# Performance work log

Measured on AMD Instinct MI355X. Metric: run time of the kernel, lower is better.

The kernel has to match this reference:

```python
import jax, jax.numpy as jnp
import numpy as np

B, D, OUT, K = 2048, 256, 256, 16


def setup_inputs() -> dict:
    key = jax.random.key(0)
    k1, k2, k3, k4 = jax.random.split(key, 4)
    x = jax.random.normal(k1, (B, D), dtype=jnp.float32)
    values = jax.random.uniform(k2, (OUT, D, K), dtype=jnp.float32, minval=-0.05, maxval=0.05)
    skip_w = jax.random.normal(k3, (OUT, D), dtype=jnp.float32) * (1.0 / np.sqrt(D).astype(np.float32))
    skip_b = jax.random.normal(k4, (OUT,), dtype=jnp.float32) * 0.01
    return {"x": x, "values": values, "skip_w": skip_w, "skip_b": skip_b}


def reference(x, values, skip_w, skip_b):
    # x: (B, D); values: (OUT, D, K); skip_w: (OUT, D); skip_b: (OUT,)
    num_knots = values.shape[-1]
    grid = jnp.linspace(-1.0, 1.0, num_knots)  # (K,)
    xc = jnp.clip(x, -1.0, 1.0)
    # torch.bucketize(x, grid) with right=False == searchsorted side='left'
    right = jnp.searchsorted(grid, xc, side='left')
    left = jnp.clip(right - 1, 0, num_knots - 2)  # (B, D)
    right = left + 1
    g0 = grid[left]
    g1 = grid[right]
    w = (xc - g0) / (g1 - g0 + 1e-12)  # (B, D)
    # Gather spline values per (sample, input-dim) knot bucket.
    vt = jnp.transpose(values, (1, 2, 0))  # (D, K, OUT)
    dim_idx = jnp.arange(xc.shape[1])[None, :]  # (1, D)
    v_left = vt[dim_idx, left]    # (B, D, OUT)
    v_right = vt[dim_idx, right]  # (B, D, OUT)
    # Linear interpolation + sum over input dims.
    y = jnp.sum((1.0 - w)[..., None] * v_left + w[..., None] * v_right, axis=1)  # (B, OUT)
    # Skip connection on the clamped input (torch reassigns x = clamp(x) first).
    return y + xc @ skip_w.T + skip_b
```

## Files before the change

### kernel.cpp

```cpp
#include <hip/hip_runtime.h>
#include <hip/hip_bf16.h>


namespace {
constexpr int Bsz  = 2048;
constexpr int Din  = 256;
constexpr int Dout = 256;
constexpr int Kn   = 16;
constexpr int KKNOT = Din * Kn;
constexpr int Ksp   = KKNOT + Din;
constexpr int KB    = Ksp / 32;
constexpr int KBK   = KKNOT / 32;
constexpr float INV_H = 7.5f;
constexpr float Hgrid = 2.0f / 15.0f;

constexpr int NSPLIT = 9;
constexpr int SPSK   = 16;
constexpr int SPSS   = 8;
constexpr int PELEM  = Bsz * Dout;
constexpr int SXS    = 36;
}

typedef __attribute__((ext_vector_type(8))) short shortx8;
typedef __attribute__((ext_vector_type(4))) float floatx4;

__device__ __forceinline__ unsigned int f2bf(float f) {
  __hip_bfloat16 h = __float2bfloat16(f);
  return (unsigned int)*reinterpret_cast<unsigned short*>(&h);
}
__device__ __forceinline__ float clamp1(float v) {
  return fminf(1.f, fmaxf(-1.f, v));
}
__device__ __forceinline__ unsigned int packbf(unsigned int e0, unsigned int e1) {
  return (e1 & 0xffff0000u) | (e0 >> 16);
}
__device__ __forceinline__ unsigned int rnd(float f) {
  return __float_as_uint(f) + 0x8000u;
}

__global__ __launch_bounds__(256) void kan_prep(
    const float* __restrict__ values, const float* __restrict__ skip_w,
    unsigned short* __restrict__ Wf) {
  const int tid = blockIdx.x * 256 + threadIdx.x;
  const int q  = tid & 3;
  const int n  = (tid >> 2) & 15;
  const int og = (tid >> 6) & 15;
  const int kb = tid >> 10;
  const int o  = og * 16 + n;
  const int k0 = kb * 32 + q * 8;
  const float* src = (kb < KBK)
      ? values + (size_t)o * KKNOT + k0
      : skip_w + (size_t)o * Din + (k0 - KKNOT);
  const float4 v0 = *(const float4*)src;
  const float4 v1 = *(const float4*)(src + 4);
  const size_t chunk = (size_t)kb * 1024 + og * 64 + q * 16 + n;
  *(uint4*)(Wf + chunk * 8) = make_uint4(
      f2bf(v0.x) | (f2bf(v0.y) << 16), f2bf(v0.z) | (f2bf(v0.w) << 16),
      f2bf(v1.x) | (f2bf(v1.y) << 16), f2bf(v1.z) | (f2bf(v1.w) << 16));
}

__global__ __launch_bounds__(256) void kan_gemm(
    const float* __restrict__ x, const unsigned short* __restrict__ Wf,
    float* __restrict__ part) {
  __shared__ float sx[32 * SXS];
  __shared__ __align__(16) unsigned short aLds[2][32 * 32];

  const int tid  = threadIdx.x;
  const int wave = tid >> 6, lane = tid & 63;
  const int ks   = blockIdx.x % NSPLIT;
  const int mi   = blockIdx.x / NSPLIT;
  const int m0   = mi * 32;
  const int og0  = wave * 4;
  const int lrow = lane & 15, lq = lane >> 4;

  const int brow = tid >> 3;
  const int bseg = tid & 7;
  const float h0 = (float)((bseg & 3) * 4);
  const int   bds = bseg >> 2;

  const uint4* B = (const uint4*)Wf;

  floatx4 acc[2][4] = {};
  uint4 bb[2][4];

  if (ks < 8) {
    const int kb0 = ks * SPSK;
    const int d0  = ks * 32;
    {
      const float4 v = *(const float4*)(x + (size_t)(m0 + brow) * Din + d0 + bseg * 4);
      *(float4*)&sx[brow * SXS + bseg * 4] = v;
    }
    __syncthreads();

    #pragma unroll
    for (int j = 0; j < 4; ++j)
      bb[0][j] = B[(size_t)kb0 * 1024 + (og0 + j) * 64 + lane];
    {
      const float xv = sx[brow * SXS + 0 + bds];
      const float t  = (clamp1(xv) + 1.f) * INV_H;
      unsigned int e0 = rnd(fmaxf(0.f, 1.f - fabsf(t - h0)));
      unsigned int e1 = rnd(fmaxf(0.f, 1.f - fabsf(t - (h0 + 1.f))));
      unsigned int e2 = rnd(fmaxf(0.f, 1.f - fabsf(t - (h0 + 2.f))));
      unsigned int e3 = rnd(fmaxf(0.f, 1.f - fabsf(t - (h0 + 3.f))));
      *(uint2*)&aLds[0][brow * 32 + bseg * 4] =
          make_uint2(packbf(e0, e1), packbf(e2, e3));
    }

    for (int s = 0; s < SPSK; ++s) {
      const int cur = s & 1, nxt = cur ^ 1;
      if (s + 1 < SPSK) {
        #pragma unroll
        for (int j = 0; j < 4; ++j)
          bb[nxt][j] = B[(size_t)(kb0 + s + 1) * 1024 + (og0 + j) * 64 + lane];
      }
      __syncthreads();

      if (s + 1 < SPSK) {
        const float xv = sx[brow * SXS + 2 * (s + 1) + bds];
        const float t  = (clamp1(xv) + 1.f) * INV_H;
        unsigned int e0 = rnd(fmaxf(0.f, 1.f - fabsf(t - h0)));
        unsigned int e1 = rnd(fmaxf(0.f, 1.f - fabsf(t - (h0 + 1.f))));
        unsigned int e2 = rnd(fmaxf(0.f, 1.f - fabsf(t - (h0 + 2.f))));
        unsigned int e3 = rnd(fmaxf(0.f, 1.f - fabsf(t - (h0 + 3.f))));
        *(uint2*)&aLds[nxt][brow * 32 + bseg * 4] =
            make_uint2(packbf(e0, e1), packbf(e2, e3));
      }

      shortx8 af[2];
      #pragma unroll
      for (int i = 0; i < 2; ++i)
        af[i] = *(const shortx8*)&aLds[cur][(16 * i + lrow) * 32 + lq * 8];
      #pragma unroll
      for (int j = 0; j < 4; ++j) {
        union { uint4 u; shortx8 s; } bc;
        bc.u = bb[cur][j];
        #pragma unroll
        for (int i = 0; i < 2; ++i)
          acc[i][j] = __builtin_amdgcn_mfma_f32_16x16x32_bf16(af[i], bc.s, acc[i][j], 0, 0, 0);
      }
    }
  } else {
    const int kb0 = KBK;
    float4 px[2];
    #pragma unroll
    for (int j = 0; j < 4; ++j)
      bb[0][j] = B[(size_t)kb0 * 1024 + (og0 + j) * 64 + lane];
    px[0] = *(const float4*)(x + (size_t)(m0 + brow) * Din + bseg * 4);
    {
      *(uint2*)&aLds[0][brow * 32 + bseg * 4] = make_uint2(
          packbf(rnd(clamp1(px[0].x)), rnd(clamp1(px[0].y))),
          packbf(rnd(clamp1(px[0].z)), rnd(clamp1(px[0].w))));
    }

    for (int s = 0; s < SPSS; ++s) {
      const int cur = s & 1, nxt = cur ^ 1;
      if (s + 1 < SPSS) {
        #pragma unroll
        for (int j = 0; j < 4; ++j)
          bb[nxt][j] = B[(size_t)(kb0 + s + 1) * 1024 + (og0 + j) * 64 + lane];
        px[nxt] = *(const float4*)(x + (size_t)(m0 + brow) * Din + (s + 1) * 32 + bseg * 4);
      }
      __syncthreads();

      if (s + 1 < SPSS) {
        *(uint2*)&aLds[nxt][brow * 32 + bseg * 4] = make_uint2(
            packbf(rnd(clamp1(px[nxt].x)), rnd(clamp1(px[nxt].y))),
            packbf(rnd(clamp1(px[nxt].z)), rnd(clamp1(px[nxt].w))));
      }

      shortx8 af[2];
      #pragma unroll
      for (int i = 0; i < 2; ++i)
        af[i] = *(const shortx8*)&aLds[cur][(16 * i + lrow) * 32 + lq * 8];
      #pragma unroll
      for (int j = 0; j < 4; ++j) {
        union { uint4 u; shortx8 s; } bc;
        bc.u = bb[cur][j];
        #pragma unroll
        for (int i = 0; i < 2; ++i)
          acc[i][j] = __builtin_amdgcn_mfma_f32_16x16x32_bf16(af[i], bc.s, acc[i][j], 0, 0, 0);
      }
    }
  }

  const int wtile = mi * 4 + wave;
  float* P = part + (size_t)ks * PELEM + (size_t)wtile * 2048;
  #pragma unroll
  for (int i = 0; i < 2; ++i)
    #pragma unroll
    for (int j = 0; j < 4; ++j)
      *(floatx4*)&P[((i * 4 + j) * 64 + lane) * 4] = acc[i][j];
}

__global__ __launch_bounds__(256) void kan_reduce(
    const float* __restrict__ part, const float* __restrict__ skip_b,
    float* __restrict__ out) {
  const int tid = blockIdx.x * 256 + threadIdx.x;
  float4 a = make_float4(0.f, 0.f, 0.f, 0.f);
  #pragma unroll
  for (int s = 0; s < NSPLIT; ++s) {
    const float4 p = *(const float4*)(part + (size_t)s * PELEM + (size_t)tid * 4);
    a.x += p.x; a.y += p.y; a.z += p.z; a.w += p.w;
  }
  const int f4    = tid & 511, wtile = tid >> 9;
  const int ij    = f4 >> 6,  lane  = f4 & 63;
  const int i     = ij >> 2,  j     = ij & 3;
  const int mi    = wtile >> 2;
  const int wave  = wtile & 3;
  const int b0    = mi * 32 + 16 * i + (lane >> 4) * 4;
  const int o     = wave * 64 + 16 * j + (lane & 15);
  const float sb  = skip_b[o];
  out[(size_t)(b0 + 0) * Dout + o] = a.x + sb;
  out[(size_t)(b0 + 1) * Dout + o] = a.y + sb;
  out[(size_t)(b0 + 2) * Dout + o] = a.z + sb;
  out[(size_t)(b0 + 3) * Dout + o] = a.w + sb;
}

__device__ __forceinline__ void knot_interp(float xraw, float& xv, float& w, int& l) {
  xv = fminf(1.0f, fmaxf(-1.0f, xraw));
  float t = (xv + 1.0f) * INV_H;
  l = (int)ceilf(t) - 1;
  l = l < 0 ? 0 : (l > Kn - 2 ? Kn - 2 : l);
  float g0 = -1.0f + Hgrid * (float)l;
  w = (xv - g0) * INV_H;
}

__global__ __launch_bounds__(256) void prep_transpose(
    const float* __restrict__ values, const float* __restrict__ skip_w,
    float* __restrict__ vt, float* __restrict__ swt) {
  int idx = blockIdx.x * blockDim.x + threadIdx.x;
  if (idx < Din * Kn * Dout) {
    int k = idx & (Kn - 1);
    int d = (idx >> 4) & (Din - 1);
    int o = idx >> 12;
    vt[(d * Kn + k) * Dout + o] = values[idx];
  }
  if (idx < Dout * Din) {
    int d = idx & (Din - 1);
    int o = idx >> 8;
    swt[d * Dout + o] = skip_w[idx];
  }
}

__global__ __launch_bounds__(256) void kan_main(
    const float* __restrict__ x, const float* __restrict__ vt,
    const float* __restrict__ swt, const float* __restrict__ skip_b,
    float* __restrict__ out) {
  __shared__ float s_w[4][Din];
  __shared__ float s_x[4][Din];
  __shared__ int   s_l[4][Din];
  const int tid = threadIdx.x;
  const int b0  = blockIdx.x * 4;
  for (int i = tid; i < 4 * Din; i += 256) {
    int bb = i >> 8;
    int d  = i & (Din - 1);
    float xv, w; int l;
    knot_interp(x[(b0 + bb) * Din + d], xv, w, l);
    s_w[bb][d] = w; s_x[bb][d] = xv; s_l[bb][d] = l;
  }
  __syncthreads();
  const int g = tid >> 6, lane = tid & 63;
  const int o = lane << 2, b = b0 + g;
  float4 acc = make_float4(0.f, 0.f, 0.f, 0.f);
  for (int d = 0; d < Din; ++d) {
    const float w = s_w[g][d], xv = s_x[g][d];
    const int l = s_l[g][d];
    const float* base = vt + (d * Kn + l) * Dout + o;
    const float4 vl = *(const float4*)(base);
    const float4 vr = *(const float4*)(base + Dout);
    const float4 sw = *(const float4*)(swt + d * Dout + o);
    acc.x = fmaf(xv, sw.x, fmaf(w, vr.x - vl.x, acc.x + vl.x));
    acc.y = fmaf(xv, sw.y, fmaf(w, vr.y - vl.y, acc.y + vl.y));
    acc.z = fmaf(xv, sw.z, fmaf(w, vr.z - vl.z, acc.z + vl.z));
    acc.w = fmaf(xv, sw.w, fmaf(w, vr.w - vl.w, acc.w + vl.w));
  }
  const float4 bias = *(const float4*)(skip_b + o);
  acc.x += bias.x; acc.y += bias.y; acc.z += bias.z; acc.w += bias.w;
  *(float4*)(out + (size_t)b * Dout + o) = acc;
}

extern "C" void kernel_launch(void* const* d_in, const int* in_sizes, int n_in,
                              void* d_out, int out_size, void* d_ws, size_t ws_size,
                              hipStream_t stream) {
  (void)in_sizes; (void)n_in; (void)out_size;
  const float* x      = (const float*)d_in[0];
  const float* values = (const float*)d_in[1];
  const float* skip_w = (const float*)d_in[2];
  const float* skip_b = (const float*)d_in[3];
  float* out = (float*)d_out;

  const size_t wf_bytes   = (size_t)Dout * Ksp * sizeof(unsigned short);
  const size_t part_bytes = (size_t)NSPLIT * PELEM * sizeof(float);
  const size_t need_gemm  = wf_bytes + part_bytes;
  const size_t need_fb    = (size_t)(Din * Kn * Dout + Din * Dout) * sizeof(float);

  if (ws_size >= need_gemm) {
    unsigned short* Wf = (unsigned short*)d_ws;
    float* part = (float*)((char*)d_ws + wf_bytes);
    kan_prep<<<(KB * 1024) / 256, 256, 0, stream>>>(values, skip_w, Wf);
    kan_gemm<<<(Bsz / 32) * NSPLIT, 256, 0, stream>>>(x, Wf, part);
    kan_reduce<<<PELEM / 4 / 256, 256, 0, stream>>>(part, skip_b, out);
  } else if (ws_size >= need_fb) {
    float* vt  = (float*)d_ws;
    float* swt = vt + Din * Kn * Dout;
    prep_transpose<<<(Din * Kn * Dout + 255) / 256, 256, 0, stream>>>(values, skip_w, vt, swt);
    kan_main<<<Bsz / 4, 256, 0, stream>>>(x, vt, swt, skip_b, out);
  }
}
```

Before: 78.24 us.

## Halve GEMM row tile and cut split-K count to reduce partial traffic

The row tile per block shrinks from 32 to 16 and the K split drops from 9 to 5, so each spline slice now covers 64 input dims. Each thread builds two hat-basis entries instead of four, and each wave issues one MFMA row tile instead of two. The aim is to shrink the partial-sum buffer written and reduced (fewer splits) while keeping the block count similar. The cost is that each weight tile loaded is reused across half as many rows, which raises weight bandwidth per output, and each K loop is longer.

```diff
diff --git a/kernel.cpp b/kernel.cpp
--- a/kernel.cpp
+++ b/kernel.cpp
@@ -14,11 +14,11 @@
 constexpr float INV_H = 7.5f;
 constexpr float Hgrid = 2.0f / 15.0f;
 
-constexpr int NSPLIT = 9;
-constexpr int SPSK   = 16;
+constexpr int NSPLIT = 5;
+constexpr int SPSK   = 32;
 constexpr int SPSS   = 8;
 constexpr int PELEM  = Bsz * Dout;
-constexpr int SXS    = 36;
+constexpr int SXS    = 68;
 }
 
 typedef __attribute__((ext_vector_type(8))) short shortx8;
@@ -62,33 +62,33 @@
 __global__ __launch_bounds__(256) void kan_gemm(
     const float* __restrict__ x, const unsigned short* __restrict__ Wf,
     float* __restrict__ part) {
-  __shared__ float sx[32 * SXS];
-  __shared__ __align__(16) unsigned short aLds[2][32 * 32];
+  __shared__ float sx[16 * SXS];
+  __shared__ __align__(16) unsigned short aLds[2][16 * 32];
 
   const int tid  = threadIdx.x;
   const int wave = tid >> 6, lane = tid & 63;
   const int ks   = blockIdx.x % NSPLIT;
   const int mi   = blockIdx.x / NSPLIT;
-  const int m0   = mi * 32;
+  const int m0   = mi * 16;
   const int og0  = wave * 4;
   const int lrow = lane & 15, lq = lane >> 4;
 
-  const int brow = tid >> 3;
-  const int bseg = tid & 7;
-  const float h0 = (float)((bseg & 3) * 4);
-  const int   bds = bseg >> 2;
+  const int brow  = tid >> 4;
+  const int bcol2 = tid & 15;
+  const int dsel  = bcol2 >> 3;
+  const float h0  = (float)(2 * (bcol2 & 7));
 
   const uint4* B = (const uint4*)Wf;
 
-  floatx4 acc[2][4] = {};
+  floatx4 acc[4] = {};
   uint4 bb[2][4];
 
-  if (ks < 8) {
+  if (ks < 4) {
     const int kb0 = ks * SPSK;
-    const int d0  = ks * 32;
+    const int d0  = ks * 64;
     {
-      const float4 v = *(const float4*)(x + (size_t)(m0 + brow) * Din + d0 + bseg * 4);
-      *(float4*)&sx[brow * SXS + bseg * 4] = v;
+      const float4 v = *(const float4*)(x + (size_t)(m0 + brow) * Din + d0 + bcol2 * 4);
+      *(float4*)&sx[brow * SXS + bcol2 * 4] = v;
     }
     __syncthreads();
 
@@ -96,14 +96,11 @@
     for (int j = 0; j < 4; ++j)
       bb[0][j] = B[(size_t)kb0 * 1024 + (og0 + j) * 64 + lane];
     {
-      const float xv = sx[brow * SXS + 0 + bds];
+      const float xv = sx[brow * SXS + dsel];
       const float t  = (clamp1(xv) + 1.f) * INV_H;
-      unsigned int e0 = rnd(fmaxf(0.f, 1.f - fabsf(t - h0)));
-      unsigned int e1 = rnd(fmaxf(0.f, 1.f - fabsf(t - (h0 + 1.f))));
-      unsigned int e2 = rnd(fmaxf(0.f, 1.f - fabsf(t - (h0 + 2.f))));
-      unsigned int e3 = rnd(fmaxf(0.f, 1.f - fabsf(t - (h0 + 3.f))));
-      *(uint2*)&aLds[0][brow * 32 + bseg * 4] =
-          make_uint2(packbf(e0, e1), packbf(e2, e3));
+      const unsigned int e0 = rnd(fmaxf(0.f, 1.f - fabsf(t - h0)));
+      const unsigned int e1 = rnd(fmaxf(0.f, 1.f - fabsf(t - (h0 + 1.f))));
+      *(unsigned int*)&aLds[0][brow * 32 + 2 * bcol2] = packbf(e0, e1);
     }
 
     for (int s = 0; s < SPSK; ++s) {
@@ -116,41 +113,30 @@
       __syncthreads();
 
       if (s + 1 < SPSK) {
-        const float xv = sx[brow * SXS + 2 * (s + 1) + bds];
+        const float xv = sx[brow * SXS + 2 * (s + 1) + dsel];
         const float t  = (clamp1(xv) + 1.f) * INV_H;
-        unsigned int e0 = rnd(fmaxf(0.f, 1.f - fabsf(t - h0)));
-        unsigned int e1 = rnd(fmaxf(0.f, 1.f - fabsf(t - (h0 + 1.f))));
-        unsigned int e2 = rnd(fmaxf(0.f, 1.f - fabsf(t - (h0 + 2.f))));
-        unsigned int e3 = rnd(fmaxf(0.f, 1.f - fabsf(t - (h0 + 3.f))));
-        *(uint2*)&aLds[nxt][brow * 32 + bseg * 4] =
-            make_uint2(packbf(e0, e1), packbf(e2, e3));
-      }
-
-      shortx8 af[2];
-      #pragma unroll
-      for (int i = 0; i < 2; ++i)
-        af[i] = *(const shortx8*)&aLds[cur][(16 * i + lrow) * 32 + lq * 8];
+        const unsigned int e0 = rnd(fmaxf(0.f, 1.f - fabsf(t - h0)));
+        const unsigned int e1 = rnd(fmaxf(0.f, 1.f - fabsf(t - (h0 + 1.f))));
+        *(unsigned int*)&aLds[nxt][brow * 32 + 2 * bcol2] = packbf(e0, e1);
+      }
+
+      const shortx8 af = *(const shortx8*)&aLds[cur][lrow * 32 + lq * 8];
       #pragma unroll
       for (int j = 0; j < 4; ++j) {
         union { uint4 u; shortx8 s; } bc;
         bc.u = bb[cur][j];
-        #pragma unroll
-        for (int i = 0; i < 2; ++i)
-          acc[i][j] = __builtin_amdgcn_mfma_f32_16x16x32_bf16(af[i], bc.s, acc[i][j], 0, 0, 0);
+        acc[j] = __builtin_amdgcn_mfma_f32_16x16x32_bf16(af, bc.s, acc[j], 0, 0, 0);
       }
     }
   } else {
     const int kb0 = KBK;
-    float4 px[2];
+    float2 px[2];
     #pragma unroll
     for (int j = 0; j < 4; ++j)
       bb[0][j] = B[(size_t)kb0 * 1024 + (og0 + j) * 64 + lane];
-    px[0] = *(const float4*)(x + (size_t)(m0 + brow) * Din + bseg * 4);
-    {
-      *(uint2*)&aLds[0][brow * 32 + bseg * 4] = make_uint2(
-          packbf(rnd(clamp1(px[0].x)), rnd(clamp1(px[0].y))),
-          packbf(rnd(clamp1(px[0].z)), rnd(clamp1(px[0].w))));
-    }
+    px[0] = *(const float2*)(x + (size_t)(m0 + brow) * Din + 2 * bcol2);
+    *(unsigned int*)&aLds[0][brow * 32 + 2 * bcol2] =
+        packbf(rnd(clamp1(px[0].x)), rnd(clamp1(px[0].y)));
 
     for (int s = 0; s < SPSS; ++s) {
       const int cur = s & 1, nxt = cur ^ 1;
@@ -158,38 +144,30 @@
         #pragma unroll
         for (int j = 0; j < 4; ++j)
           bb[nxt][j] = B[(size_t)(kb0 + s + 1) * 1024 + (og0 + j) * 64 + lane];
-        px[nxt] = *(const float4*)(x + (size_t)(m0 + brow) * Din + (s + 1) * 32 + bseg * 4);
+        px[nxt] = *(const float2*)(x + (size_t)(m0 + brow) * Din + (s + 1) * 32 + 2 * bcol2);
       }
       __syncthreads();
 
       if (s + 1 < SPSS) {
-        *(uint2*)&aLds[nxt][brow * 32 + bseg * 4] = make_uint2(
-            packbf(rnd(clamp1(px[nxt].x)), rnd(clamp1(px[nxt].y))),
-            packbf(rnd(clamp1(px[nxt].z)), rnd(clamp1(px[nxt].w))));
-      }
-
-      shortx8 af[2];
-      #pragma unroll
-      for (int i = 0; i < 2; ++i)
-        af[i] = *(const shortx8*)&aLds[cur][(16 * i + lrow) * 32 + lq * 8];
+        *(unsigned int*)&aLds[nxt][brow * 32 + 2 * bcol2] =
+            packbf(rnd(clamp1(px[nxt].x)), rnd(clamp1(px[nxt].y)));
+      }
+
+      const shortx8 af = *(const shortx8*)&aLds[cur][lrow * 32 + lq * 8];
       #pragma unroll
       for (int j = 0; j < 4; ++j) {
         union { uint4 u; shortx8 s; } bc;
         bc.u = bb[cur][j];
-        #pragma unroll
-        for (int i = 0; i < 2; ++i)
-          acc[i][j] = __builtin_amdgcn_mfma_f32_16x16x32_bf16(af[i], bc.s, acc[i][j], 0, 0, 0);
+        acc[j] = __builtin_amdgcn_mfma_f32_16x16x32_bf16(af, bc.s, acc[j], 0, 0, 0);
       }
     }
   }
 
   const int wtile = mi * 4 + wave;
-  float* P = part + (size_t)ks * PELEM + (size_t)wtile * 2048;
+  float* P = part + (size_t)ks * PELEM + (size_t)wtile * 1024;
   #pragma unroll
-  for (int i = 0; i < 2; ++i)
-    #pragma unroll
-    for (int j = 0; j < 4; ++j)
-      *(floatx4*)&P[((i * 4 + j) * 64 + lane) * 4] = acc[i][j];
+  for (int j = 0; j < 4; ++j)
+    *(floatx4*)&P[(j * 64 + lane) * 4] = acc[j];
 }
 
 __global__ __launch_bounds__(256) void kan_reduce(
@@ -202,13 +180,12 @@
     const float4 p = *(const float4*)(part + (size_t)s * PELEM + (size_t)tid * 4);
     a.x += p.x; a.y += p.y; a.z += p.z; a.w += p.w;
   }
-  const int f4    = tid & 511, wtile = tid >> 9;
-  const int ij    = f4 >> 6,  lane  = f4 & 63;
-  const int i     = ij >> 2,  j     = ij & 3;
+  const int f4    = tid & 255, wtile = tid >> 8;
+  const int j     = f4 >> 6,  lane  = f4 & 63;
   const int mi    = wtile >> 2;
   const int wave  = wtile & 3;
-  const int b0    = mi * 32 + 16 * i + (lane >> 4) * 4;
-  const int o     = wave * 64 + 16 * j + (lane & 15);
+  const int b0    = mi * 16 + (lane >> 4) * 4;
+  const int o     = wave * 64 + j * 16 + (lane & 15);
   const float sb  = skip_b[o];
   out[(size_t)(b0 + 0) * Dout + o] = a.x + sb;
   out[(size_t)(b0 + 1) * Dout + o] = a.y + sb;
@@ -298,7 +275,7 @@
     unsigned short* Wf = (unsigned short*)d_ws;
     float* part = (float*)((char*)d_ws + wf_bytes);
     kan_prep<<<(KB * 1024) / 256, 256, 0, stream>>>(values, skip_w, Wf);
-    kan_gemm<<<(Bsz / 32) * NSPLIT, 256, 0, stream>>>(x, Wf, part);
+    kan_gemm<<<(Bsz / 16) * NSPLIT, 256, 0, stream>>>(x, Wf, part);
     kan_reduce<<<PELEM / 4 / 256, 256, 0, stream>>>(part, skip_b, out);
   } else if (ws_size >= need_fb) {
     float* vt  = (float*)d_ws;
```

New measurement: 82.20 us. +5.1%, slower.
